# Kernel optimization log

Measured on AMD Instinct MI355X. Metric: run time of the kernel, lower is better.

The kernel has to match this reference:

```python
import jax, jax.numpy as jnp
import numpy as np

N0 = 100000
N1 = 100000
K = 16
D_MODEL = 64
D_ATTN = 32
H = 4


def setup_inputs() -> dict:
    key = jax.random.key(0)
    ks = jax.random.split(key, 12)
    inp = {
        "coords0": jax.random.normal(ks[0], (N0, 3), jnp.float32),
        "coords1": jax.random.normal(ks[1], (N1, 3), jnp.float32),
        "feats0": jax.random.normal(ks[2], (N0, D_MODEL), jnp.float32),
        "feats1": jax.random.normal(ks[3], (N1, D_MODEL), jnp.float32),
        "knn_idxs": jax.random.randint(ks[4], (1, N1, K), 0, N0, jnp.int64 if jax.config.jax_enable_x64 else jnp.int32),
        # Linear params (PyTorch Linear: y = x @ W.T + b; stored here already transposed as [in, out])
        "Wq": jax.random.normal(ks[5], (D_MODEL, D_ATTN), jnp.float32) / np.sqrt(D_MODEL),
        "bq": jnp.zeros((D_ATTN,), jnp.float32),
        "Wk": jax.random.normal(ks[6], (D_MODEL + 3, D_ATTN), jnp.float32) / np.sqrt(D_MODEL + 3),
        "bk": jnp.zeros((D_ATTN,), jnp.float32),
        "Wv": jax.random.normal(ks[7], (D_MODEL + 3, D_MODEL), jnp.float32) / np.sqrt(D_MODEL + 3),
        "bv": jnp.zeros((D_MODEL,), jnp.float32),
    }
    return inp


def reference(coords0, coords1, feats0, feats1, knn_idxs, Wq, bq, Wk, bk, Wv, bv):
    idx = knn_idxs[0]  # [N1, K] neighbor indices into cloud 0
    n1, k_ = idx.shape
    dh_attn = D_ATTN // H   # per-head query/key depth
    dh_val = D_MODEL // H   # per-head value depth

    # Irregular gathers from source cloud
    g_feats = feats0[idx]                         # [N1, K, D_MODEL]
    rel = coords0[idx] - coords1[:, None, :]      # [N1, K, 3] relative coords
    kv_in = jnp.concatenate([g_feats, rel], axis=-1)  # [N1, K, D_MODEL+3]

    # Projections + head split
    q = (feats1 @ Wq + bq).reshape(n1, H, dh_attn)                    # [N1, H, dh]
    k = (kv_in @ Wk + bk).reshape(n1, k_, H, dh_attn).transpose(0, 2, 1, 3)  # [N1, H, K, dh]
    v = (kv_in @ Wv + bv).reshape(n1, k_, H, dh_val).transpose(0, 2, 1, 3)   # [N1, H, K, dv]

    # Attention over K neighbors per point
    attn = jnp.einsum('nhd,nhkd->nhk', q, k) / np.sqrt(dh_attn).astype(np.float32)
    attn = jax.nn.softmax(attn, axis=-1)          # [N1, H, K]
    out = jnp.einsum('nhk,nhkd->nhd', attn, v)    # [N1, H, dv]
    out = out.reshape(n1, -1)                     # [N1, D_MODEL]
    return out, knn_idxs
```

## Files before the change

kernel.cpp:

```cpp
#include <hip/hip_runtime.h>


using half8  = __attribute__((ext_vector_type(8))) _Float16;
using half4  = __attribute__((ext_vector_type(4))) _Float16;
using floatx4 = __attribute__((ext_vector_type(4))) float;

__global__ __launch_bounds__(256) void frag_setup_kernel(
    const float* __restrict__ Wq, const float* __restrict__ Wk,
    const float* __restrict__ Wv,
    _Float16* __restrict__ fragKV, _Float16* __restrict__ fragQ)
{
    const int stride = blockDim.x * gridDim.x;
    for (int e = blockIdx.x * blockDim.x + threadIdx.x; e < 6 * 2 * 64 * 8; e += stride) {
        int j = e & 7, lane = (e >> 3) & 63, h = (e >> 9) & 1, t = e >> 10;
        int k = h * 32 + ((lane >> 4) * 8) + j;
        int n = t * 16 + (lane & 15);
        float v = (n < 32) ? Wk[k * 32 + n] : Wv[k * 64 + (n - 32)];
        fragKV[e] = (_Float16)v;
    }
    for (int e = blockIdx.x * blockDim.x + threadIdx.x; e < 2 * 2 * 64 * 8; e += stride) {
        int j = e & 7, lane = (e >> 3) & 63, h = (e >> 9) & 1, t = e >> 10;
        int k = h * 32 + ((lane >> 4) * 8) + j;
        int n = t * 16 + (lane & 15);
        fragQ[e] = (_Float16)Wq[k * 32 + n];
    }
}

template <int NT, bool F16OUT>
__global__ __launch_bounds__(256, 4) void proj_kernel(
    const float* __restrict__ X, const _Float16* __restrict__ frag,
    const float* __restrict__ bA, const float* __restrict__ bB, int split,
    void* __restrict__ outv, int nrows)
{
    const int tid  = threadIdx.x;
    const int wave = tid >> 6;
    const int lane = tid & 63;
    const int l15  = lane & 15;
    const int quad = lane >> 4;
    const int m0   = blockIdx.x * 64 + wave * 16;

    const int row  = m0 + l15;
    const int rowc = (row < nrows) ? row : 0;

    const floatx4* X4 = (const floatx4*)(X + (size_t)rowc * 64);
    floatx4 f0 = X4[quad * 2 + 0], f1 = X4[quad * 2 + 1];
    floatx4 f2 = X4[quad * 2 + 8], f3 = X4[quad * 2 + 9];

    half8 a0, a1;
    a0[0] = (_Float16)f0.x; a0[1] = (_Float16)f0.y; a0[2] = (_Float16)f0.z; a0[3] = (_Float16)f0.w;
    a0[4] = (_Float16)f1.x; a0[5] = (_Float16)f1.y; a0[6] = (_Float16)f1.z; a0[7] = (_Float16)f1.w;
    a1[0] = (_Float16)f2.x; a1[1] = (_Float16)f2.y; a1[2] = (_Float16)f2.z; a1[3] = (_Float16)f2.w;
    a1[4] = (_Float16)f3.x; a1[5] = (_Float16)f3.y; a1[6] = (_Float16)f3.z; a1[7] = (_Float16)f3.w;

    const half8* bf = (const half8*)frag;

    floatx4 acc[NT];
    #pragma unroll
    for (int t = 0; t < NT; t++) {
        int n = t * 16 + l15;
        float bb = (n < split) ? bA[n] : bB[n - split];
        acc[t] = (floatx4){bb, bb, bb, bb};
    }
    #pragma unroll
    for (int t = 0; t < NT; t++) {
        acc[t] = __builtin_amdgcn_mfma_f32_16x16x32_f16(a0, bf[(t * 2 + 0) * 64 + lane], acc[t], 0, 0, 0);
        acc[t] = __builtin_amdgcn_mfma_f32_16x16x32_f16(a1, bf[(t * 2 + 1) * 64 + lane], acc[t], 0, 0, 0);
    }

    const int NCOL = NT * 16;
    #pragma unroll
    for (int t = 0; t < NT; t++) {
        #pragma unroll
        for (int r = 0; r < 4; r++) {
            int ro = m0 + quad * 4 + r;
            if (ro < nrows) {
                if (F16OUT) ((_Float16*)outv)[(size_t)ro * NCOL + t * 16 + l15] = (_Float16)acc[t][r];
                else        ((float*)outv)   [(size_t)ro * NCOL + t * 16 + l15] = acc[t][r];
            }
        }
    }
}

__global__ __launch_bounds__(256, 4) void attn_kernel(
    const float* __restrict__ coords0, const float* __restrict__ coords1,
    const int*   __restrict__ knn,
    const float* __restrict__ Qf, const _Float16* __restrict__ KVh,
    const float* __restrict__ Wk, const float* __restrict__ Wv,
    float* __restrict__ out, float* __restrict__ outIdx, int n1)
{
    __shared__ float sWk3[3][32];
    __shared__ __align__(16) float sWv3[3][64];
    __shared__ __align__(16) float sAttn[16][68];
    __shared__ float sRel[16][16][3];
    __shared__ int   sIdx[16][16];

    const int tid = threadIdx.x;
    if (tid < 96)  ((float*)sWk3)[tid] = Wk[64 * 32 + tid];
    if (tid < 192) ((float*)sWv3)[tid] = Wv[64 * 64 + tid];
    __syncthreads();

    const int p = tid >> 4;
    const int j = tid & 15;
    const int n = blockIdx.x * 16 + p;
    const bool valid = (n < n1);
    const int nc = valid ? n : (n1 - 1);

    const int idx = knn[nc * 16 + j];
    const float c1x = coords1[nc * 3 + 0];
    const float c1y = coords1[nc * 3 + 1];
    const float c1z = coords1[nc * 3 + 2];
    const float r0 = coords0[idx * 3 + 0] - c1x;
    const float r1 = coords0[idx * 3 + 1] - c1y;
    const float r2 = coords0[idx * 3 + 2] - c1z;

    const half8*   kr = (const half8*)(KVh + (size_t)idx * 96);
    const floatx4* qr = (const floatx4*)(Qf + (size_t)nc * 32);

    float logit[4];
    #pragma unroll
    for (int h = 0; h < 4; h++) {
        half8 k8 = kr[h];
        floatx4 q0 = qr[h * 2 + 0], q1 = qr[h * 2 + 1];
        float qv[8] = {q0.x, q0.y, q0.z, q0.w, q1.x, q1.y, q1.z, q1.w};
        float acc = 0.f;
        #pragma unroll
        for (int i = 0; i < 8; i++) {
            int d = h * 8 + i;
            float kk = fmaf(r0, sWk3[0][d],
                       fmaf(r1, sWk3[1][d],
                       fmaf(r2, sWk3[2][d], (float)k8[i])));
            acc = fmaf(qv[i], kk, acc);
        }
        logit[h] = acc;
    }

    const float scale = 0.35355339059327373f;
    #pragma unroll
    for (int h = 0; h < 4; h++) {
        float l = logit[h] * scale;
        float m = l;
        m = fmaxf(m, __shfl_xor(m, 1, 16));
        m = fmaxf(m, __shfl_xor(m, 2, 16));
        m = fmaxf(m, __shfl_xor(m, 4, 16));
        m = fmaxf(m, __shfl_xor(m, 8, 16));
        float e = __expf(l - m);
        float s = e;
        s += __shfl_xor(s, 1, 16);
        s += __shfl_xor(s, 2, 16);
        s += __shfl_xor(s, 4, 16);
        s += __shfl_xor(s, 8, 16);
        sAttn[p][h * 16 + j] = e * __builtin_amdgcn_rcpf(s);
    }
    sRel[p][j][0] = r0; sRel[p][j][1] = r1; sRel[p][j][2] = r2;
    sIdx[p][j] = idx;

    if (valid) outIdx[n * 16 + j] = (float)idx;

    __syncthreads();

    const int hh = j >> 2;
    float a_[16];
    int   iv_[16];
    #pragma unroll
    for (int t = 0; t < 4; t++) {
        ((floatx4*)a_)[t] = ((const floatx4*)&sAttn[p][hh * 16])[t];
        ((int4*)iv_)[t]   = ((const int4*)&sIdx[p][0])[t];
    }

    floatx4 accA = {0.f, 0.f, 0.f, 0.f}, accB = {0.f, 0.f, 0.f, 0.f};
    float rb0 = 0.f, rb1 = 0.f, rb2 = 0.f;
    #pragma unroll
    for (int jj = 0; jj < 16; jj += 2) {
        half4 v0 = *(const half4*)(KVh + (size_t)iv_[jj]     * 96 + 32 + j * 4);
        half4 v1 = *(const half4*)(KVh + (size_t)iv_[jj + 1] * 96 + 32 + j * 4);
        float aA = a_[jj], aB = a_[jj + 1];
        accA.x = fmaf(aA, (float)v0[0], accA.x);
        accA.y = fmaf(aA, (float)v0[1], accA.y);
        accA.z = fmaf(aA, (float)v0[2], accA.z);
        accA.w = fmaf(aA, (float)v0[3], accA.w);
        accB.x = fmaf(aB, (float)v1[0], accB.x);
        accB.y = fmaf(aB, (float)v1[1], accB.y);
        accB.z = fmaf(aB, (float)v1[2], accB.z);
        accB.w = fmaf(aB, (float)v1[3], accB.w);
        rb0 = fmaf(aA, sRel[p][jj][0], rb0); rb0 = fmaf(aB, sRel[p][jj + 1][0], rb0);
        rb1 = fmaf(aA, sRel[p][jj][1], rb1); rb1 = fmaf(aB, sRel[p][jj + 1][1], rb1);
        rb2 = fmaf(aA, sRel[p][jj][2], rb2); rb2 = fmaf(aB, sRel[p][jj + 1][2], rb2);
    }

    floatx4 wa = ((const floatx4*)&sWv3[0][0])[j];
    floatx4 wb = ((const floatx4*)&sWv3[1][0])[j];
    floatx4 wc = ((const floatx4*)&sWv3[2][0])[j];
    floatx4 acc;
    acc.x = accA.x + accB.x + rb0 * wa.x + rb1 * wb.x + rb2 * wc.x;
    acc.y = accA.y + accB.y + rb0 * wa.y + rb1 * wb.y + rb2 * wc.y;
    acc.z = accA.z + accB.z + rb0 * wa.z + rb1 * wb.z + rb2 * wc.z;
    acc.w = accA.w + accB.w + rb0 * wa.w + rb1 * wb.w + rb2 * wc.w;

    if (valid) ((floatx4*)out)[n * 16 + j] = acc;
}

extern "C" void kernel_launch(void* const* d_in, const int* in_sizes, int n_in,
                              void* d_out, int out_size, void* d_ws, size_t ws_size,
                              hipStream_t stream) {
    const float* coords0 = (const float*)d_in[0];
    const float* coords1 = (const float*)d_in[1];
    const float* feats0  = (const float*)d_in[2];
    const float* feats1  = (const float*)d_in[3];
    const int*   knn     = (const int*)d_in[4];
    const float* Wq      = (const float*)d_in[5];
    const float* bq      = (const float*)d_in[6];
    const float* Wk      = (const float*)d_in[7];
    const float* bk      = (const float*)d_in[8];
    const float* Wv      = (const float*)d_in[9];
    const float* bv      = (const float*)d_in[10];

    const int n0 = in_sizes[0] / 3;
    const int n1 = in_sizes[1] / 3;

    char* ws = (char*)d_ws;
    _Float16* fragKV = (_Float16*)(ws + 0);
    _Float16* fragQ  = (_Float16*)(ws + 16384);
    _Float16* KVh    = (_Float16*)(ws + 32768);
    float*    Qf     = (float*)(ws + 32768 + (size_t)n0 * 96 * 2 + 64);
    Qf = (float*)(((size_t)Qf + 15) & ~(size_t)15);

    float* out    = (float*)d_out;
    float* outIdx = out + (size_t)n1 * 64;

    frag_setup_kernel<<<16, 256, 0, stream>>>(Wq, Wk, Wv, fragKV, fragQ);
    proj_kernel<6, true ><<<(n0 + 63) / 64, 256, 0, stream>>>(feats0, fragKV, bk, bv, 32, (void*)KVh, n0);
    proj_kernel<2, false><<<(n1 + 63) / 64, 256, 0, stream>>>(feats1, fragQ, bq, bq, 999, (void*)Qf, n1);
    attn_kernel<<<(n1 + 15) / 16, 256, 0, stream>>>(coords0, coords1, knn,
                                                    Qf, KVh, Wk, Wv, out, outIdx, n1);
}
```

Before: 199.9 us.

## Fuse projection kernels and restructure neighbor attention loads and softmax

Merges the weight-fragment setup and the K/V and Q projection launches into one kernel. Each block now rebuilds the MFMA weight fragments in shared memory, and the K/V output is staged through LDS so global stores are coalesced. In the attention kernel, Q is staged in shared memory and q·Wk for the coordinate rows is precomputed per head, so relative coordinates add via three FMAs instead of per-dimension work. V gathers become 16-byte loads split across half-groups and combined with shuffles. The softmax max-subtraction is dropped, which saves shuffles but risks overflow if logits get large. Rebuilding the fragments in every block adds redundant weight reads.

Measured after the change: 200.6 us. Within noise of the previous version (+0.3%).

```diff
diff --git a/kernel.cpp b/kernel.cpp
--- a/kernel.cpp
+++ b/kernel.cpp
@@ -1,83 +1,118 @@
 #include <hip/hip_runtime.h>
 
 
-using half8  = __attribute__((ext_vector_type(8))) _Float16;
-using half4  = __attribute__((ext_vector_type(4))) _Float16;
+using half8   = __attribute__((ext_vector_type(8))) _Float16;
+using half4   = __attribute__((ext_vector_type(4))) _Float16;
 using floatx4 = __attribute__((ext_vector_type(4))) float;
 
-__global__ __launch_bounds__(256) void frag_setup_kernel(
-    const float* __restrict__ Wq, const float* __restrict__ Wk,
-    const float* __restrict__ Wv,
-    _Float16* __restrict__ fragKV, _Float16* __restrict__ fragQ)
+__global__ __launch_bounds__(256, 4) void proj_fused(
+    const float* __restrict__ feats0, const float* __restrict__ feats1,
+    const float* __restrict__ Wq, const float* __restrict__ bq,
+    const float* __restrict__ Wk, const float* __restrict__ bk,
+    const float* __restrict__ Wv, const float* __restrict__ bv,
+    _Float16* __restrict__ KVh, float* __restrict__ Qf,
+    int n0, int n1, int nb0)
 {
-    const int stride = blockDim.x * gridDim.x;
-    for (int e = blockIdx.x * blockDim.x + threadIdx.x; e < 6 * 2 * 64 * 8; e += stride) {
-        int j = e & 7, lane = (e >> 3) & 63, h = (e >> 9) & 1, t = e >> 10;
-        int k = h * 32 + ((lane >> 4) * 8) + j;
-        int n = t * 16 + (lane & 15);
-        float v = (n < 32) ? Wk[k * 32 + n] : Wv[k * 64 + (n - 32)];
-        fragKV[e] = (_Float16)v;
-    }
-    for (int e = blockIdx.x * blockDim.x + threadIdx.x; e < 2 * 2 * 64 * 8; e += stride) {
-        int j = e & 7, lane = (e >> 3) & 63, h = (e >> 9) & 1, t = e >> 10;
-        int k = h * 32 + ((lane >> 4) * 8) + j;
-        int n = t * 16 + (lane & 15);
-        fragQ[e] = (_Float16)Wq[k * 32 + n];
-    }
-}
-
-template <int NT, bool F16OUT>
-__global__ __launch_bounds__(256, 4) void proj_kernel(
-    const float* __restrict__ X, const _Float16* __restrict__ frag,
-    const float* __restrict__ bA, const float* __restrict__ bB, int split,
-    void* __restrict__ outv, int nrows)
-{
+    __shared__ __align__(16) _Float16 sFrag[6144];
+    __shared__ __align__(16) _Float16 sOut[6144];
+
     const int tid  = threadIdx.x;
     const int wave = tid >> 6;
     const int lane = tid & 63;
     const int l15  = lane & 15;
     const int quad = lane >> 4;
-    const int m0   = blockIdx.x * 64 + wave * 16;
-
-    const int row  = m0 + l15;
-    const int rowc = (row < nrows) ? row : 0;
-
-    const floatx4* X4 = (const floatx4*)(X + (size_t)rowc * 64);
-    floatx4 f0 = X4[quad * 2 + 0], f1 = X4[quad * 2 + 1];
-    floatx4 f2 = X4[quad * 2 + 8], f3 = X4[quad * 2 + 9];
-
-    half8 a0, a1;
-    a0[0] = (_Float16)f0.x; a0[1] = (_Float16)f0.y; a0[2] = (_Float16)f0.z; a0[3] = (_Float16)f0.w;
-    a0[4] = (_Float16)f1.x; a0[5] = (_Float16)f1.y; a0[6] = (_Float16)f1.z; a0[7] = (_Float16)f1.w;
-    a1[0] = (_Float16)f2.x; a1[1] = (_Float16)f2.y; a1[2] = (_Float16)f2.z; a1[3] = (_Float16)f2.w;
-    a1[4] = (_Float16)f3.x; a1[5] = (_Float16)f3.y; a1[6] = (_Float16)f3.z; a1[7] = (_Float16)f3.w;
-
-    const half8* bf = (const half8*)frag;
-
-    floatx4 acc[NT];
-    #pragma unroll
-    for (int t = 0; t < NT; t++) {
-        int n = t * 16 + l15;
-        float bb = (n < split) ? bA[n] : bB[n - split];
-        acc[t] = (floatx4){bb, bb, bb, bb};
-    }
-    #pragma unroll
-    for (int t = 0; t < NT; t++) {
-        acc[t] = __builtin_amdgcn_mfma_f32_16x16x32_f16(a0, bf[(t * 2 + 0) * 64 + lane], acc[t], 0, 0, 0);
-        acc[t] = __builtin_amdgcn_mfma_f32_16x16x32_f16(a1, bf[(t * 2 + 1) * 64 + lane], acc[t], 0, 0, 0);
-    }
-
-    const int NCOL = NT * 16;
-    #pragma unroll
-    for (int t = 0; t < NT; t++) {
-        #pragma unroll
-        for (int r = 0; r < 4; r++) {
-            int ro = m0 + quad * 4 + r;
-            if (ro < nrows) {
-                if (F16OUT) ((_Float16*)outv)[(size_t)ro * NCOL + t * 16 + l15] = (_Float16)acc[t][r];
-                else        ((float*)outv)   [(size_t)ro * NCOL + t * 16 + l15] = acc[t][r];
+
+    if ((int)blockIdx.x < nb0) {
+        const int rowBase = blockIdx.x * 64;
+        for (int e = tid; e < 6144; e += 256) {
+            int j = e & 7, ln = (e >> 3) & 63, h = (e >> 9) & 1, t = e >> 10;
+            int k = h * 32 + ((ln >> 4) * 8) + j;
+            int n = t * 16 + (ln & 15);
+            float v = (n < 32) ? Wk[k * 32 + n] : Wv[k * 64 + (n - 32)];
+            sFrag[e] = (_Float16)v;
+        }
+        __syncthreads();
+
+        const int m0   = rowBase + wave * 16;
+        const int row  = m0 + l15;
+        const int rowc = (row < n0) ? row : (n0 - 1);
+        const floatx4* X4 = (const floatx4*)(feats0 + (size_t)rowc * 64);
+        floatx4 f0 = X4[quad * 2 + 0], f1 = X4[quad * 2 + 1];
+        floatx4 f2 = X4[quad * 2 + 8], f3 = X4[quad * 2 + 9];
+        half8 a0, a1;
+        a0[0]=(_Float16)f0.x; a0[1]=(_Float16)f0.y; a0[2]=(_Float16)f0.z; a0[3]=(_Float16)f0.w;
+        a0[4]=(_Float16)f1.x; a0[5]=(_Float16)f1.y; a0[6]=(_Float16)f1.z; a0[7]=(_Float16)f1.w;
+        a1[0]=(_Float16)f2.x; a1[1]=(_Float16)f2.y; a1[2]=(_Float16)f2.z; a1[3]=(_Float16)f2.w;
+        a1[4]=(_Float16)f3.x; a1[5]=(_Float16)f3.y; a1[6]=(_Float16)f3.z; a1[7]=(_Float16)f3.w;
+
+        const half8* bf = (const half8*)sFrag;
+        floatx4 acc[6];
+        #pragma unroll
+        for (int t = 0; t < 6; t++) {
+            int n = t * 16 + l15;
+            float bb = (n < 32) ? bk[n] : bv[n - 32];
+            acc[t] = (floatx4){bb, bb, bb, bb};
+        }
+        #pragma unroll
+        for (int t = 0; t < 6; t++) {
+            acc[t] = __builtin_amdgcn_mfma_f32_16x16x32_f16(a0, bf[(t*2+0)*64 + lane], acc[t], 0,0,0);
+            acc[t] = __builtin_amdgcn_mfma_f32_16x16x32_f16(a1, bf[(t*2+1)*64 + lane], acc[t], 0,0,0);
+        }
+
+        #pragma unroll
+        for (int t = 0; t < 6; t++)
+            #pragma unroll
+            for (int r = 0; r < 4; r++)
+                sOut[(wave * 16 + quad * 4 + r) * 96 + t * 16 + l15] = (_Float16)acc[t][r];
+        __syncthreads();
+
+        const half8* so8 = (const half8*)sOut;
+        half8* dst = (half8*)(KVh + (size_t)rowBase * 96);
+        for (int c = tid; c < 768; c += 256) {
+            int r = c / 12;
+            if (rowBase + r < n0) dst[c] = so8[c];
+        }
+    } else {
+        const int rowBase = ((int)blockIdx.x - nb0) * 64;
+        for (int e = tid; e < 2048; e += 256) {
+            int j = e & 7, ln = (e >> 3) & 63, h = (e >> 9) & 1, t = e >> 10;
+            int k = h * 32 + ((ln >> 4) * 8) + j;
+            int n = t * 16 + (ln & 15);
+            sFrag[e] = (_Float16)Wq[k * 32 + n];
+        }
+        __syncthreads();
+
+        const int m0   = rowBase + wave * 16;
+        const int row  = m0 + l15;
+        const int rowc = (row < n1) ? row : (n1 - 1);
+        const floatx4* X4 = (const floatx4*)(feats1 + (size_t)rowc * 64);
+        floatx4 f0 = X4[quad * 2 + 0], f1 = X4[quad * 2 + 1];
+        floatx4 f2 = X4[quad * 2 + 8], f3 = X4[quad * 2 + 9];
+        half8 a0, a1;
+        a0[0]=(_Float16)f0.x; a0[1]=(_Float16)f0.y; a0[2]=(_Float16)f0.z; a0[3]=(_Float16)f0.w;
+        a0[4]=(_Float16)f1.x; a0[5]=(_Float16)f1.y; a0[6]=(_Float16)f1.z; a0[7]=(_Float16)f1.w;
+        a1[0]=(_Float16)f2.x; a1[1]=(_Float16)f2.y; a1[2]=(_Float16)f2.z; a1[3]=(_Float16)f2.w;
+        a1[4]=(_Float16)f3.x; a1[5]=(_Float16)f3.y; a1[6]=(_Float16)f3.z; a1[7]=(_Float16)f3.w;
+
+        const half8* bf = (const half8*)sFrag;
+        floatx4 acc[2];
+        #pragma unroll
+        for (int t = 0; t < 2; t++) {
+            float bb = bq[t * 16 + l15];
+            acc[t] = (floatx4){bb, bb, bb, bb};
+        }
+        #pragma unroll
+        for (int t = 0; t < 2; t++) {
+            acc[t] = __builtin_amdgcn_mfma_f32_16x16x32_f16(a0, bf[(t*2+0)*64 + lane], acc[t], 0,0,0);
+            acc[t] = __builtin_amdgcn_mfma_f32_16x16x32_f16(a1, bf[(t*2+1)*64 + lane], acc[t], 0,0,0);
+        }
+        #pragma unroll
+        for (int t = 0; t < 2; t++)
+            #pragma unroll
+            for (int r = 0; r < 4; r++) {
+                int ro = m0 + quad * 4 + r;
+                if (ro < n1) Qf[(size_t)ro * 32 + t * 16 + l15] = acc[t][r];
             }
-        }
     }
 }
 
@@ -88,15 +123,24 @@
     const float* __restrict__ Wk, const float* __restrict__ Wv,
     float* __restrict__ out, float* __restrict__ outIdx, int n1)
 {
+    __shared__ __align__(16) float sQ[16][36];
     __shared__ float sWk3[3][32];
-    __shared__ __align__(16) float sWv3[3][64];
-    __shared__ __align__(16) float sAttn[16][68];
+    __shared__ float sWv3[3][64];
+    __shared__ float sAttn[16][4][18];
     __shared__ float sRel[16][16][3];
     __shared__ int   sIdx[16][16];
 
     const int tid = threadIdx.x;
-    if (tid < 96)  ((float*)sWk3)[tid] = Wk[64 * 32 + tid];
-    if (tid < 192) ((float*)sWv3)[tid] = Wv[64 * 64 + tid];
+    for (int e = tid; e < 288; e += 256) {
+        if (e < 96) ((float*)sWk3)[e] = Wk[2048 + e];
+        else        ((float*)sWv3)[e - 96] = Wv[4096 + (e - 96)];
+    }
+    if (tid < 128) {
+        int pt = tid >> 3, c4 = tid & 7;
+        int r = blockIdx.x * 16 + pt;
+        if (r >= n1) r = n1 - 1;
+        ((floatx4*)&sQ[pt][0])[c4] = ((const floatx4*)Qf)[(size_t)r * 8 + c4];
+    }
     __syncthreads();
 
     const int p = tid >> 4;
@@ -106,97 +150,99 @@
     const int nc = valid ? n : (n1 - 1);
 
     const int idx = knn[nc * 16 + j];
-    const float c1x = coords1[nc * 3 + 0];
-    const float c1y = coords1[nc * 3 + 1];
-    const float c1z = coords1[nc * 3 + 2];
-    const float r0 = coords0[idx * 3 + 0] - c1x;
-    const float r1 = coords0[idx * 3 + 1] - c1y;
-    const float r2 = coords0[idx * 3 + 2] - c1z;
-
-    const half8*   kr = (const half8*)(KVh + (size_t)idx * 96);
-    const floatx4* qr = (const floatx4*)(Qf + (size_t)nc * 32);
-
-    float logit[4];
+    const half8* kr = (const half8*)(KVh + (size_t)idx * 96);
+    half8 k8[4];
+    #pragma unroll
+    for (int h = 0; h < 4; h++) k8[h] = kr[h];
+
+    const float r0 = coords0[idx * 3 + 0] - coords1[nc * 3 + 0];
+    const float r1 = coords0[idx * 3 + 1] - coords1[nc * 3 + 1];
+    const float r2 = coords0[idx * 3 + 2] - coords1[nc * 3 + 2];
+
+    float t_own = 0.f;
+    if (j < 12) {
+        int c = j >> 2, h = j & 3;
+        #pragma unroll
+        for (int i = 0; i < 8; i++)
+            t_own = fmaf(sWk3[c][h * 8 + i], sQ[p][h * 8 + i], t_own);
+    }
+    float tt[3][4];
+    #pragma unroll
+    for (int c = 0; c < 3; c++)
+        #pragma unroll
+        for (int h = 0; h < 4; h++)
+            tt[c][h] = __shfl(t_own, c * 4 + h, 16);
+
+    const float scale = 0.35355339059327373f;
     #pragma unroll
     for (int h = 0; h < 4; h++) {
-        half8 k8 = kr[h];
-        floatx4 q0 = qr[h * 2 + 0], q1 = qr[h * 2 + 1];
-        float qv[8] = {q0.x, q0.y, q0.z, q0.w, q1.x, q1.y, q1.z, q1.w};
-        float acc = 0.f;
-        #pragma unroll
-        for (int i = 0; i < 8; i++) {
-            int d = h * 8 + i;
-            float kk = fmaf(r0, sWk3[0][d],
-                       fmaf(r1, sWk3[1][d],
-                       fmaf(r2, sWk3[2][d], (float)k8[i])));
-            acc = fmaf(qv[i], kk, acc);
-        }
-        logit[h] = acc;
-    }
-
-    const float scale = 0.35355339059327373f;
-    #pragma unroll
-    for (int h = 0; h < 4; h++) {
-        float l = logit[h] * scale;
-        float m = l;
-        m = fmaxf(m, __shfl_xor(m, 1, 16));
-        m = fmaxf(m, __shfl_xor(m, 2, 16));
-        m = fmaxf(m, __shfl_xor(m, 4, 16));
-        m = fmaxf(m, __shfl_xor(m, 8, 16));
-        float e = __expf(l - m);
+        floatx4 q0 = ((const floatx4*)&sQ[p][0])[h * 2 + 0];
+        floatx4 q1 = ((const floatx4*)&sQ[p][0])[h * 2 + 1];
+        float acc = r0 * tt[0][h] + r1 * tt[1][h] + r2 * tt[2][h];
+        acc = fmaf(q0.x, (float)k8[h][0], acc);
+        acc = fmaf(q0.y, (float)k8[h][1], acc);
+        acc = fmaf(q0.z, (float)k8[h][2], acc);
+        acc = fmaf(q0.w, (float)k8[h][3], acc);
+        acc = fmaf(q1.x, (float)k8[h][4], acc);
+        acc = fmaf(q1.y, (float)k8[h][5], acc);
+        acc = fmaf(q1.z, (float)k8[h][6], acc);
+        acc = fmaf(q1.w, (float)k8[h][7], acc);
+        float e = __expf(acc * scale);
         float s = e;
         s += __shfl_xor(s, 1, 16);
         s += __shfl_xor(s, 2, 16);
         s += __shfl_xor(s, 4, 16);
         s += __shfl_xor(s, 8, 16);
-        sAttn[p][h * 16 + j] = e * __builtin_amdgcn_rcpf(s);
+        sAttn[p][h][j] = e * __builtin_amdgcn_rcpf(s);
     }
     sRel[p][j][0] = r0; sRel[p][j][1] = r1; sRel[p][j][2] = r2;
     sIdx[p][j] = idx;
-
     if (valid) outIdx[n * 16 + j] = (float)idx;
 
     __syncthreads();
 
-    const int hh = j >> 2;
-    float a_[16];
-    int   iv_[16];
-    #pragma unroll
-    for (int t = 0; t < 4; t++) {
-        ((floatx4*)a_)[t] = ((const floatx4*)&sAttn[p][hh * 16])[t];
-        ((int4*)iv_)[t]   = ((const int4*)&sIdx[p][0])[t];
-    }
-
-    floatx4 accA = {0.f, 0.f, 0.f, 0.f}, accB = {0.f, 0.f, 0.f, 0.f};
+    const int g = j & 7;
+    const int hf = j >> 3;
+    const int h = g >> 1;
+
+    int   iv[8];
+    float av[8];
+    #pragma unroll
+    for (int s = 0; s < 8; s++) {
+        iv[s] = sIdx[p][2 * s + hf];
+        av[s] = sAttn[p][h][2 * s + hf];
+    }
+    half8 v8[8];
+    #pragma unroll
+    for (int s = 0; s < 8; s++)
+        v8[s] = *(const half8*)(KVh + (size_t)iv[s] * 96 + 32 + g * 8);
+
+    float acc8[8] = {0,0,0,0,0,0,0,0};
     float rb0 = 0.f, rb1 = 0.f, rb2 = 0.f;
     #pragma unroll
-    for (int jj = 0; jj < 16; jj += 2) {
-        half4 v0 = *(const half4*)(KVh + (size_t)iv_[jj]     * 96 + 32 + j * 4);
-        half4 v1 = *(const half4*)(KVh + (size_t)iv_[jj + 1] * 96 + 32 + j * 4);
-        float aA = a_[jj], aB = a_[jj + 1];
-        accA.x = fmaf(aA, (float)v0[0], accA.x);
-        accA.y = fmaf(aA, (float)v0[1], accA.y);
-        accA.z = fmaf(aA, (float)v0[2], accA.z);
-        accA.w = fmaf(aA, (float)v0[3], accA.w);
-        accB.x = fmaf(aB, (float)v1[0], accB.x);
-        accB.y = fmaf(aB, (float)v1[1], accB.y);
-        accB.z = fmaf(aB, (float)v1[2], accB.z);
-        accB.w = fmaf(aB, (float)v1[3], accB.w);
-        rb0 = fmaf(aA, sRel[p][jj][0], rb0); rb0 = fmaf(aB, sRel[p][jj + 1][0], rb0);
-        rb1 = fmaf(aA, sRel[p][jj][1], rb1); rb1 = fmaf(aB, sRel[p][jj + 1][1], rb1);
-        rb2 = fmaf(aA, sRel[p][jj][2], rb2); rb2 = fmaf(aB, sRel[p][jj + 1][2], rb2);
-    }
-
-    floatx4 wa = ((const floatx4*)&sWv3[0][0])[j];
-    floatx4 wb = ((const floatx4*)&sWv3[1][0])[j];
-    floatx4 wc = ((const floatx4*)&sWv3[2][0])[j];
-    floatx4 acc;
-    acc.x = accA.x + accB.x + rb0 * wa.x + rb1 * wb.x + rb2 * wc.x;
-    acc.y = accA.y + accB.y + rb0 * wa.y + rb1 * wb.y + rb2 * wc.y;
-    acc.z = accA.z + accB.z + rb0 * wa.z + rb1 * wb.z + rb2 * wc.z;
-    acc.w = accA.w + accB.w + rb0 * wa.w + rb1 * wb.w + rb2 * wc.w;
-
-    if (valid) ((floatx4*)out)[n * 16 + j] = acc;
+    for (int s = 0; s < 8; s++) {
+        float a = av[s];
+        #pragma unroll
+        for (int i = 0; i < 8; i++)
+            acc8[i] = fmaf(a, (float)v8[s][i], acc8[i]);
+        rb0 = fmaf(a, sRel[p][2 * s + hf][0], rb0);
+        rb1 = fmaf(a, sRel[p][2 * s + hf][1], rb1);
+        rb2 = fmaf(a, sRel[p][2 * s + hf][2], rb2);
+    }
+    #pragma unroll
+    for (int i = 0; i < 8; i++) acc8[i] += __shfl_xor(acc8[i], 8, 16);
+    rb0 += __shfl_xor(rb0, 8, 16);
+    rb1 += __shfl_xor(rb1, 8, 16);
+    rb2 += __shfl_xor(rb2, 8, 16);
+
+    #pragma unroll
+    for (int i = 0; i < 8; i++)
+        acc8[i] += rb0 * sWv3[0][8 * g + i] + rb1 * sWv3[1][8 * g + i] + rb2 * sWv3[2][8 * g + i];
+
+    if (valid) {
+        floatx4 st = { acc8[hf * 4 + 0], acc8[hf * 4 + 1], acc8[hf * 4 + 2], acc8[hf * 4 + 3] };
+        ((floatx4*)out)[(size_t)n * 16 + g * 2 + hf] = st;
+    }
 }
 
 extern "C" void kernel_launch(void* const* d_in, const int* in_sizes, int n_in,
@@ -218,18 +264,17 @@
     const int n1 = in_sizes[1] / 3;
 
     char* ws = (char*)d_ws;
-    _Float16* fragKV = (_Float16*)(ws + 0);
-    _Float16* fragQ  = (_Float16*)(ws + 16384);
-    _Float16* KVh    = (_Float16*)(ws + 32768);
-    float*    Qf     = (float*)(ws + 32768 + (size_t)n0 * 96 * 2 + 64);
-    Qf = (float*)(((size_t)Qf + 15) & ~(size_t)15);
+    _Float16* KVh = (_Float16*)ws;
+    float*    Qf  = (float*)(ws + (size_t)n0 * 96 * 2);
 
     float* out    = (float*)d_out;
     float* outIdx = out + (size_t)n1 * 64;
 
-    frag_setup_kernel<<<16, 256, 0, stream>>>(Wq, Wk, Wv, fragKV, fragQ);
-    proj_kernel<6, true ><<<(n0 + 63) / 64, 256, 0, stream>>>(feats0, fragKV, bk, bv, 32, (void*)KVh, n0);
-    proj_kernel<2, false><<<(n1 + 63) / 64, 256, 0, stream>>>(feats1, fragQ, bq, bq, 999, (void*)Qf, n1);
+    const int nb0 = (n0 + 63) / 64;
+    const int nb1 = (n1 + 63) / 64;
+
+    proj_fused<<<nb0 + nb1, 256, 0, stream>>>(feats0, feats1, Wq, bq, Wk, bk, Wv, bv,
+                                              KVh, Qf, n0, n1, nb0);
     attn_kernel<<<(n1 + 15) / 16, 256, 0, stream>>>(coords0, coords1, knn,
                                                     Qf, KVh, Wk, Wv, out, outIdx, n1);
 }
```
